# Kernel tuning notes

Measured on AMD Instinct MI355X. Metric: run time of the kernel, lower is better.

Reference implementation:

```python
import jax, jax.numpy as jnp
import numpy as np

N_NODES = 20000
STEPS = 10  # message_passing_steps


def _mlp(x, p):
    # 3-layer MLP: Linear->ReLU->Linear->ReLU->Linear (no final activation)
    W1, b1, W2, b2, W3, b3 = p
    h = jax.nn.relu(x @ W1 + b1)
    h = jax.nn.relu(h @ W2 + b2)
    return h @ W3 + b3


def _aggregate(dst, edge_attr, num_nodes):
    # scatter_add of edge features into destination nodes, degree-normalized (deg clamped to >=1)
    agg = jax.ops.segment_sum(edge_attr, dst, num_segments=num_nodes)
    deg = jax.ops.segment_sum(jnp.ones((dst.shape[0], 1), edge_attr.dtype), dst, num_segments=num_nodes)
    return agg / jnp.maximum(deg, 1.0)


def setup_inputs() -> dict:
    key = jax.random.key(0)
    N, EM, EC = N_NODES, 120000, 20000
    ND, MD, CD, OD, L = 12, 7, 4, 3, 128
    keys = iter(jax.random.split(key, 128))

    def lin(i, o):
        return (jax.random.normal(next(keys), (i, o), jnp.float32) * 0.05,
                jax.random.normal(next(keys), (o,), jnp.float32) * 0.05)

    inp = {
        "node_x": jax.random.normal(next(keys), (N, ND), jnp.float32),
        "mesh_edge_attr": jax.random.normal(next(keys), (EM, MD), jnp.float32),
        "contact_edge_attr": jax.random.normal(next(keys), (EC, CD), jnp.float32),
    }
    dims = {"ne": (ND, L), "me": (MD, L), "ce": (CD, L), "pe": (3 * L, L), "pn": (3 * L, L), "de": (L, OD)}
    for name, (i, o) in dims.items():
        W1, b1 = lin(i, L)
        W2, b2 = lin(L, L)
        W3, b3 = lin(L, o)
        for pn, p in zip(["W1", "b1", "W2", "b2", "W3", "b3"], [W1, b1, W2, b2, W3, b3]):
            inp[name + "_" + pn] = p
    inp["mesh_edge_index"] = jax.random.randint(next(keys), (2, EM), 0, N)
    inp["contact_edge_index"] = jax.random.randint(next(keys), (2, EC), 0, N)
    return inp


def reference(node_x, mesh_edge_attr, contact_edge_attr,
              ne_W1, ne_b1, ne_W2, ne_b2, ne_W3, ne_b3,
              me_W1, me_b1, me_W2, me_b2, me_W3, me_b3,
              ce_W1, ce_b1, ce_W2, ce_b2, ce_W3, ce_b3,
              pe_W1, pe_b1, pe_W2, pe_b2, pe_W3, pe_b3,
              pn_W1, pn_b1, pn_W2, pn_b2, pn_W3, pn_b3,
              de_W1, de_b1, de_W2, de_b2, de_W3, de_b3,
              mesh_edge_index, contact_edge_index):
    ne = (ne_W1, ne_b1, ne_W2, ne_b2, ne_W3, ne_b3)
    mep = (me_W1, me_b1, me_W2, me_b2, me_W3, me_b3)
    cep = (ce_W1, ce_b1, ce_W2, ce_b2, ce_W3, ce_b3)
    pe = (pe_W1, pe_b1, pe_W2, pe_b2, pe_W3, pe_b3)
    pn = (pn_W1, pn_b1, pn_W2, pn_b2, pn_W3, pn_b3)
    de = (de_W1, de_b1, de_W2, de_b2, de_W3, de_b3)
    N = node_x.shape[0]
    # encode
    x = _mlp(node_x, ne)                 # [N, 128]
    me = _mlp(mesh_edge_attr, mep)       # [EM, 128]
    ce = _mlp(contact_edge_attr, cep)    # [EC, 128]
    msrc, mdst = mesh_edge_index[0], mesh_edge_index[1]
    csrc, cdst = contact_edge_index[0], contact_edge_index[1]
    # process (shared edge_mlp for both edge types, residual updates)
    for _ in range(STEPS):
        me = me + _mlp(jnp.concatenate([x[msrc], x[mdst], me], axis=-1), pe)
        ce = ce + _mlp(jnp.concatenate([x[csrc], x[cdst], ce], axis=-1), pe)
        agg_m = _aggregate(mdst, me, N)
        agg_c = _aggregate(cdst, ce, N)
        x = x + _mlp(jnp.concatenate([x, agg_m, agg_c], axis=-1), pn)
    # decode
    return _mlp(x, de)                   # [N, 3]
```

## Files before the change

kernel.cpp:

```cpp
#include <hip/hip_runtime.h>
#include <stdint.h>

typedef unsigned short u16;
typedef __attribute__((ext_vector_type(8))) short bf16x8;
typedef __attribute__((ext_vector_type(4))) float f32x4;

#define NNODES 20000
#define EM 120000
#define EC 20000
#define LDIM 128
#define MT 32
#define MT2 64
#define A_STR 392
#define H_STR 136

__device__ __forceinline__ u16 f2bf(float f){
  uint32_t b = __float_as_uint(f);
  b += 0x7FFF + ((b >> 16) & 1);
  return (u16)(b >> 16);
}

template<int KB>
__device__ __forceinline__ void layer(const u16* sIn, int in_str, const u16* Wp,
                                      int wr, int wc, int lane, f32x4 acc[4]){
  const int row = wr*16 + (lane & 15);
  const int kg  = lane >> 4;
  #pragma unroll
  for (int kb = 0; kb < KB; ++kb){
    bf16x8 a = *(const bf16x8*)(sIn + row*in_str + kb*32 + kg*8);
    const u16* wb = Wp + (((kb*8 + wc*4)*64 + lane) << 3);
    #pragma unroll
    for (int nf = 0; nf < 4; ++nf){
      bf16x8 b = *(const bf16x8*)(wb + (nf << 9));
      acc[nf] = __builtin_amdgcn_mfma_f32_16x16x32_bf16(a, b, acc[nf], 0, 0, 0);
    }
  }
}

__device__ __forceinline__ void hid_epi(f32x4 acc[4], const float* bias,
                                        int wr, int wc, int lane, u16* sOut){
  const int cl = lane & 15;
  const int r0 = wr*16 + (lane >> 4)*4;
  #pragma unroll
  for (int nf = 0; nf < 4; ++nf){
    int col = wc*64 + nf*16 + cl;
    float bv = bias[col];
    #pragma unroll
    for (int r = 0; r < 4; ++r){
      float v = acc[nf][r] + bv;
      sOut[(r0 + r)*H_STR + col] = f2bf(v > 0.f ? v : 0.f);
    }
  }
}

__device__ __forceinline__ void zero4(f32x4 acc[4]){
  const f32x4 vz = {0.f, 0.f, 0.f, 0.f};
  #pragma unroll
  for (int i = 0; i < 4; ++i) acc[i] = vz;
}

template<int KB>
__device__ __forceinline__ void layer64(const u16* sIn, const u16* Wp,
                                        int wr, int wc, int lane, f32x4 acc[2][2]){
  const int r0 = wr*32 + (lane & 15);
  const int kg = lane >> 4;
  const u16* a0p = sIn + r0*A_STR + kg*8;
  const u16* a1p = a0p + 16*A_STR;
  const u16* wb  = Wp + (((wc*2)*64 + lane) << 3);
  #pragma unroll
  for (int kb = 0; kb < KB; ++kb){
    bf16x8 a0 = *(const bf16x8*)(a0p + kb*32);
    bf16x8 a1 = *(const bf16x8*)(a1p + kb*32);
    const u16* wk = wb + kb*4096;
    bf16x8 b0 = *(const bf16x8*)(wk);
    bf16x8 b1 = *(const bf16x8*)(wk + 512);
    acc[0][0] = __builtin_amdgcn_mfma_f32_16x16x32_bf16(a0, b0, acc[0][0], 0, 0, 0);
    acc[1][0] = __builtin_amdgcn_mfma_f32_16x16x32_bf16(a1, b0, acc[1][0], 0, 0, 0);
    acc[0][1] = __builtin_amdgcn_mfma_f32_16x16x32_bf16(a0, b1, acc[0][1], 0, 0, 0);
    acc[1][1] = __builtin_amdgcn_mfma_f32_16x16x32_bf16(a1, b1, acc[1][1], 0, 0, 0);
  }
}

__device__ __forceinline__ void hid_epi64(f32x4 acc[2][2], const float* bias,
                                          int wr, int wc, int lane, u16* sOut){
  const int cl = lane & 15;
  const int rq = (lane >> 4)*4;
  #pragma unroll
  for (int rf = 0; rf < 2; ++rf){
    int r0 = wr*32 + rf*16 + rq;
    #pragma unroll
    for (int nf = 0; nf < 2; ++nf){
      int col = wc*32 + nf*16 + cl;
      float bv = bias[col];
      #pragma unroll
      for (int r = 0; r < 4; ++r){
        float v = acc[rf][nf][r] + bv;
        sOut[(r0 + r)*A_STR + col] = f2bf(v > 0.f ? v : 0.f);
      }
    }
  }
}

__device__ __forceinline__ void zero22(f32x4 acc[2][2]){
  const f32x4 vz = {0.f, 0.f, 0.f, 0.f};
  acc[0][0] = vz; acc[0][1] = vz; acc[1][0] = vz; acc[1][1] = vz;
}

struct PackDesc { const float* src; int K_raw, N_raw, NF, elem_off; };
struct PackArgs { PackDesc d[18]; int total; };

__global__ __launch_bounds__(256) void pack_weights(PackArgs pa, u16* dst){
  int idx = blockIdx.x*256 + threadIdx.x;
  if (idx >= pa.total) return;
  int di = 0;
  #pragma unroll
  for (int i = 1; i < 18; ++i) if (idx >= pa.d[i].elem_off) di = i;
  PackDesc dd = pa.d[di];
  int e = idx - dd.elem_off;
  int f = e >> 9, lane = (e >> 3) & 63, j = e & 7;
  int kb = f / dd.NF, nf = f % dd.NF;
  int k = kb*32 + (lane >> 4)*8 + j;
  int n = nf*16 + (lane & 15);
  float v = (k < dd.K_raw && n < dd.N_raw) ? dd.src[k*dd.N_raw + n] : 0.f;
  dst[idx] = f2bf(v);
}

__global__ __launch_bounds__(256) void hist_kernel(const int* mdst, const int* cdst,
                                                   int* cnt_m, int* cnt_c){
  int i = blockIdx.x*256 + threadIdx.x;
  if (i < EM) atomicAdd(&cnt_m[mdst[i]], 1);
  else if (i < EM + EC) atomicAdd(&cnt_c[cdst[i - EM]], 1);
}

struct ScanArgs { const int *cnt_m, *cnt_c; int *start_m, *start_c, *cur_m, *cur_c; };

__global__ __launch_bounds__(256) void scan_kernel(ScanArgs a){
  const int n = NNODES;
  const int* cnt = blockIdx.x == 0 ? a.cnt_m : a.cnt_c;
  int* start     = blockIdx.x == 0 ? a.start_m : a.start_c;
  int* cur       = blockIdx.x == 0 ? a.cur_m : a.cur_c;
  __shared__ int part[256];
  __shared__ int base[257];
  int t = threadIdx.x;
  const int per = (n + 255) / 256;
  int lo = t*per, hi = min(n, lo + per);
  int s = 0;
  for (int j = lo; j < hi; ++j) s += cnt[j];
  part[t] = s;
  __syncthreads();
  if (t == 0){
    int run = 0;
    for (int i = 0; i < 256; ++i){ base[i] = run; run += part[i]; }
    base[256] = run;
  }
  __syncthreads();
  int run = base[t];
  for (int j = lo; j < hi; ++j){ start[j] = run; cur[j] = run; run += cnt[j]; }
  if (t == 255) start[n] = base[256];
}

__global__ __launch_bounds__(256) void scatter_kernel(const int* mdst, const int* cdst,
                                                      int* cur_m, int* cur_c,
                                                      int* eid_m, int* eid_c){
  int i = blockIdx.x*256 + threadIdx.x;
  if (i < EM){
    int p = atomicAdd(&cur_m[mdst[i]], 1);
    eid_m[p] = i;
  } else if (i < EM + EC){
    int e = i - EM;
    int p = atomicAdd(&cur_c[cdst[e]], 1);
    eid_c[p] = e;
  }
}

struct EncArgs {
  const float* in; int Kraw;
  const u16 *Wp1, *Wp2, *Wp3;
  const float *b1, *b2, *b3;
  float* out_f32; u16* out_b16;
};

__global__ __launch_bounds__(256) void enc_kernel(EncArgs a){
  __shared__ u16 sA[MT*A_STR];
  __shared__ u16 sH[MT*H_STR];
  const int tid = threadIdx.x, lane = tid & 63, w = tid >> 6, wr = w & 1, wc = w >> 1;
  const int m0 = blockIdx.x * MT;
  for (int i = tid; i < MT*32; i += 256){
    int row = i >> 5, c = i & 31;
    float v = (c < a.Kraw) ? a.in[(size_t)(m0 + row)*a.Kraw + c] : 0.f;
    sA[row*A_STR + c] = f2bf(v);
  }
  __syncthreads();
  f32x4 acc[4]; zero4(acc);
  layer<1>(sA, A_STR, a.Wp1, wr, wc, lane, acc);
  hid_epi(acc, a.b1, wr, wc, lane, sH);
  __syncthreads();
  zero4(acc);
  layer<4>(sH, H_STR, a.Wp2, wr, wc, lane, acc);
  hid_epi(acc, a.b2, wr, wc, lane, sA);
  __syncthreads();
  zero4(acc);
  layer<4>(sA, H_STR, a.Wp3, wr, wc, lane, acc);
  const int cl = lane & 15, r0l = wr*16 + (lane >> 4)*4;
  #pragma unroll
  for (int nf = 0; nf < 4; ++nf){
    int col = wc*64 + nf*16 + cl;
    float bv = a.b3[col];
    #pragma unroll
    for (int r = 0; r < 4; ++r){
      int m = m0 + r0l + r;
      float v = acc[nf][r] + bv;
      a.out_f32[(size_t)m*LDIM + col] = v;
      a.out_b16[(size_t)m*LDIM + col] = f2bf(v);
    }
  }
}

struct EdgeArgs {
  const u16 *Wp1, *Wp2, *Wp3;
  const float *b1, *b2, *b3;
  const u16* x_b16;
  const int *msrc, *mdst, *csrc, *cdst;
  u16 *me_b16, *ce_b16;
  float *me_f32, *ce_f32;
  int mesh_blocks;
};

__global__ __launch_bounds__(512) void edge_kernel(EdgeArgs a){
  __shared__ u16 sA[MT2*A_STR];
  const int tid = threadIdx.x, lane = tid & 63, w = tid >> 6, wr = w & 1, wc = w >> 1;
  const bool mesh = (int)blockIdx.x < a.mesh_blocks;
  const int e0 = (mesh ? (int)blockIdx.x : (int)blockIdx.x - a.mesh_blocks) * MT2;
  const int E = mesh ? EM : EC;
  const int* src = mesh ? a.msrc : a.csrc;
  const int* dst = mesh ? a.mdst : a.cdst;
  u16* fb   = mesh ? a.me_b16 : a.ce_b16;
  float* ff = mesh ? a.me_f32 : a.ce_f32;

  for (int i = tid; i < MT2*48; i += 512){
    int row = i/48, ch = i%48;
    int e = e0 + row; if (e >= E) e = E - 1;
    const u16* sp;
    if (ch < 16)       sp = a.x_b16 + (size_t)src[e]*LDIM + ch*8;
    else if (ch < 32)  sp = a.x_b16 + (size_t)dst[e]*LDIM + (ch-16)*8;
    else               sp = fb + (size_t)e*LDIM + (ch-32)*8;
    *(bf16x8*)(sA + row*A_STR + ch*8) = *(const bf16x8*)sp;
  }
  __syncthreads();
  f32x4 acc[2][2]; zero22(acc);
  layer64<12>(sA, a.Wp1, wr, wc, lane, acc);
  __syncthreads();
  hid_epi64(acc, a.b1, wr, wc, lane, sA + 256);
  __syncthreads();
  zero22(acc);
  layer64<4>(sA + 256, a.Wp2, wr, wc, lane, acc);
  hid_epi64(acc, a.b2, wr, wc, lane, sA);
  __syncthreads();
  zero22(acc);
  layer64<4>(sA, a.Wp3, wr, wc, lane, acc);

  const int cl = lane & 15, rq = (lane >> 4)*4;
  #pragma unroll
  for (int rf = 0; rf < 2; ++rf){
    #pragma unroll
    for (int r = 0; r < 4; ++r){
      int e = e0 + wr*32 + rf*16 + rq + r;
      if (e < E){
        #pragma unroll
        for (int nf = 0; nf < 2; ++nf){
          int col = wc*32 + nf*16 + cl;
          float nv = ff[(size_t)e*LDIM + col] + acc[rf][nf][r] + a.b3[col];
          ff[(size_t)e*LDIM + col] = nv;
          fb[(size_t)e*LDIM + col] = f2bf(nv);
        }
      }
    }
  }
}

struct NodeArgs {
  const u16 *Wp1, *Wp2, *Wp3;
  const float *b1, *b2, *b3;
  const u16* x_b16_in;
  const float *me_f32, *ce_f32;
  const int *start_m, *eid_m, *start_c, *eid_c;
  float* x_f32; u16* x_b16_out;
};

__global__ __launch_bounds__(512) void node_kernel(NodeArgs a){
  __shared__ u16 sA[MT2*A_STR];
  const int tid = threadIdx.x, lane = tid & 63, w = tid >> 6, wr = w & 1, wc = w >> 1;
  const int n0 = blockIdx.x * MT2;

  for (int i = tid; i < MT2*16; i += 512){
    int row = i >> 4, ch = i & 15;
    int n = n0 + row; if (n >= NNODES) n = NNODES - 1;
    *(bf16x8*)(sA + row*A_STR + ch*8) = *(const bf16x8*)(a.x_b16_in + (size_t)n*LDIM + ch*8);
  }

  {
    const int r = tid >> 3, c0 = (tid & 7) * 16;
    const int n = n0 + r;
    const bool ok = n < NNODES;
    {
      int s = ok ? a.start_m[n] : 0, e = ok ? a.start_m[n+1] : 0;
      f32x4 a0{0,0,0,0}, a1{0,0,0,0}, a2{0,0,0,0}, a3{0,0,0,0};
      for (int j = s; j < e; ++j){
        const f32x4* p = (const f32x4*)(a.me_f32 + (size_t)a.eid_m[j]*LDIM + c0);
        a0 += p[0]; a1 += p[1]; a2 += p[2]; a3 += p[3];
      }
      float inv = 1.f / fmaxf((float)(e - s), 1.f);
      bf16x8 t0, t1;
      #pragma unroll
      for (int k = 0; k < 4; ++k){
        t0[k]   = (short)f2bf(a0[k]*inv); t0[k+4] = (short)f2bf(a1[k]*inv);
        t1[k]   = (short)f2bf(a2[k]*inv); t1[k+4] = (short)f2bf(a3[k]*inv);
      }
      *(bf16x8*)(sA + r*A_STR + 128 + c0) = t0;
      *(bf16x8*)(sA + r*A_STR + 128 + c0 + 8) = t1;
    }
    {
      int s = ok ? a.start_c[n] : 0, e = ok ? a.start_c[n+1] : 0;
      f32x4 a0{0,0,0,0}, a1{0,0,0,0}, a2{0,0,0,0}, a3{0,0,0,0};
      for (int j = s; j < e; ++j){
        const f32x4* p = (const f32x4*)(a.ce_f32 + (size_t)a.eid_c[j]*LDIM + c0);
        a0 += p[0]; a1 += p[1]; a2 += p[2]; a3 += p[3];
      }
      float inv = 1.f / fmaxf((float)(e - s), 1.f);
      bf16x8 t0, t1;
      #pragma unroll
      for (int k = 0; k < 4; ++k){
        t0[k]   = (short)f2bf(a0[k]*inv); t0[k+4] = (short)f2bf(a1[k]*inv);
        t1[k]   = (short)f2bf(a2[k]*inv); t1[k+4] = (short)f2bf(a3[k]*inv);
      }
      *(bf16x8*)(sA + r*A_STR + 256 + c0) = t0;
      *(bf16x8*)(sA + r*A_STR + 256 + c0 + 8) = t1;
    }
  }
  __syncthreads();
  f32x4 acc[2][2]; zero22(acc);
  layer64<12>(sA, a.Wp1, wr, wc, lane, acc);
  __syncthreads();
  hid_epi64(acc, a.b1, wr, wc, lane, sA + 256);
  __syncthreads();
  zero22(acc);
  layer64<4>(sA + 256, a.Wp2, wr, wc, lane, acc);
  hid_epi64(acc, a.b2, wr, wc, lane, sA);
  __syncthreads();
  zero22(acc);
  layer64<4>(sA, a.Wp3, wr, wc, lane, acc);

  const int cl = lane & 15, rq = (lane >> 4)*4;
  #pragma unroll
  for (int rf = 0; rf < 2; ++rf){
    #pragma unroll
    for (int r = 0; r < 4; ++r){
      int n = n0 + wr*32 + rf*16 + rq + r;
      if (n < NNODES){
        #pragma unroll
        for (int nf = 0; nf < 2; ++nf){
          int col = wc*32 + nf*16 + cl;
          float nv = a.x_f32[(size_t)n*LDIM + col] + acc[rf][nf][r] + a.b3[col];
          a.x_f32[(size_t)n*LDIM + col] = nv;
          a.x_b16_out[(size_t)n*LDIM + col] = f2bf(nv);
        }
      }
    }
  }
}

struct DecArgs {
  const u16 *Wp1, *Wp2, *Wp3;
  const float *b1, *b2, *b3;
  const u16* x_b16; float* out;
};

__global__ __launch_bounds__(256) void dec_kernel(DecArgs a){
  __shared__ u16 sA[MT*A_STR];
  __shared__ u16 sH[MT*H_STR];
  const int tid = threadIdx.x, lane = tid & 63, w = tid >> 6, wr = w & 1, wc = w >> 1;
  const int n0 = blockIdx.x * MT;
  for (int i = tid; i < MT*16; i += 256){
    int row = i >> 4, ch = i & 15;
    *(bf16x8*)(sA + row*H_STR + ch*8) = *(const bf16x8*)(a.x_b16 + (size_t)(n0+row)*LDIM + ch*8);
  }
  __syncthreads();
  f32x4 acc[4]; zero4(acc);
  layer<4>(sA, H_STR, a.Wp1, wr, wc, lane, acc);
  hid_epi(acc, a.b1, wr, wc, lane, sH);
  __syncthreads();
  zero4(acc);
  layer<4>(sH, H_STR, a.Wp2, wr, wc, lane, acc);
  hid_epi(acc, a.b2, wr, wc, lane, sA);
  __syncthreads();
  if (wc == 0){
    f32x4 a3 = {0.f, 0.f, 0.f, 0.f};
    const int row = wr*16 + (lane & 15), kg = lane >> 4;
    #pragma unroll
    for (int kb = 0; kb < 4; ++kb){
      bf16x8 av = *(const bf16x8*)(sA + row*H_STR + kb*32 + kg*8);
      bf16x8 bv = *(const bf16x8*)(a.Wp3 + ((kb*64 + lane) << 3));
      a3 = __builtin_amdgcn_mfma_f32_16x16x32_bf16(av, bv, a3, 0, 0, 0);
    }
    const int cl = lane & 15, r0l = wr*16 + (lane >> 4)*4;
    if (cl < 3){
      #pragma unroll
      for (int r = 0; r < 4; ++r)
        a.out[(size_t)(n0 + r0l + r)*3 + cl] = a3[r] + a.b3[cl];
    }
  }
}

extern "C" void kernel_launch(void* const* d_in, const int* in_sizes, int n_in,
                              void* d_out, int out_size, void* d_ws, size_t ws_size,
                              hipStream_t stream){
  auto F = [&](int i){ return (const float*)d_in[i]; };
  const float* node_x   = F(0);
  const float* mesh_attr = F(1);
  const float* cont_attr = F(2);
  const int* mei = (const int*)d_in[39];
  const int* cei = (const int*)d_in[40];
  const int *msrc = mei, *mdst = mei + EM, *csrc = cei, *cdst = cei + EC;

  char* ws = (char*)d_ws;
  size_t off = 0;
  auto take = [&](size_t b)->void*{ void* p = ws + off; off += (b + 255) & ~(size_t)255; return p; };
  float* x_f32  = (float*)take((size_t)NNODES*LDIM*4);
  u16*   x_b16  = (u16*)  take((size_t)NNODES*LDIM*2);
  float* me_f32 = (float*)take((size_t)EM*LDIM*4);
  u16*   me_b16 = (u16*)  take((size_t)EM*LDIM*2);
  float* ce_f32 = (float*)take((size_t)EC*LDIM*4);
  u16*   ce_b16 = (u16*)  take((size_t)EC*LDIM*2);
  u16*   wpack  = (u16*)  take((size_t)309248*2);
  int* cnt_m   = (int*)take((size_t)NNODES*4);
  int* cnt_c   = (int*)take((size_t)NNODES*4);
  int* start_m = (int*)take((size_t)(NNODES+1)*4);
  int* start_c = (int*)take((size_t)(NNODES+1)*4);
  int* cur_m   = (int*)take((size_t)NNODES*4);
  int* cur_c   = (int*)take((size_t)NNODES*4);
  int* eid_m   = (int*)take((size_t)EM*4);
  int* eid_c   = (int*)take((size_t)EC*4);

  static const int tbl[18][5] = {
    {3,12,128,32,128},{5,128,128,128,128},{7,128,128,128,128},
    {9,7,128,32,128},{11,128,128,128,128},{13,128,128,128,128},
    {15,4,128,32,128},{17,128,128,128,128},{19,128,128,128,128},
    {21,384,128,384,128},{23,128,128,128,128},{25,128,128,128,128},
    {27,384,128,384,128},{29,128,128,128,128},{31,128,128,128,128},
    {33,128,128,128,128},{35,128,128,128,128},{37,128,3,128,16}};
  PackArgs pa; int eo = 0; int offs[18];
  for (int i = 0; i < 18; ++i){
    offs[i] = eo;
    pa.d[i].src = F(tbl[i][0]);
    pa.d[i].K_raw = tbl[i][1];
    pa.d[i].N_raw = tbl[i][2];
    pa.d[i].NF = tbl[i][4] / 16;
    pa.d[i].elem_off = eo;
    eo += tbl[i][3] * tbl[i][4];
  }
  pa.total = eo;
  pack_weights<<<dim3(eo/256), dim3(256), 0, stream>>>(pa, wpack);

  size_t cnt_span = ((char*)cnt_c - (char*)cnt_m) + (size_t)NNODES*4;
  hipMemsetAsync(cnt_m, 0, cnt_span, stream);
  hist_kernel<<<dim3((EM + EC + 255)/256), dim3(256), 0, stream>>>(mdst, cdst, cnt_m, cnt_c);
  ScanArgs sa{cnt_m, cnt_c, start_m, start_c, cur_m, cur_c};
  scan_kernel<<<dim3(2), dim3(256), 0, stream>>>(sa);
  scatter_kernel<<<dim3((EM + EC + 255)/256), dim3(256), 0, stream>>>(mdst, cdst, cur_m, cur_c, eid_m, eid_c);

  EncArgs en{node_x, 12, wpack+offs[0], wpack+offs[1], wpack+offs[2], F(4), F(6), F(8), x_f32, x_b16};
  enc_kernel<<<dim3(NNODES/MT), dim3(256), 0, stream>>>(en);
  EncArgs em{mesh_attr, 7, wpack+offs[3], wpack+offs[4], wpack+offs[5], F(10), F(12), F(14), me_f32, me_b16};
  enc_kernel<<<dim3(EM/MT), dim3(256), 0, stream>>>(em);
  EncArgs ec{cont_attr, 4, wpack+offs[6], wpack+offs[7], wpack+offs[8], F(16), F(18), F(20), ce_f32, ce_b16};
  enc_kernel<<<dim3(EC/MT), dim3(256), 0, stream>>>(ec);

  EdgeArgs ea;
  ea.Wp1 = wpack+offs[9]; ea.Wp2 = wpack+offs[10]; ea.Wp3 = wpack+offs[11];
  ea.b1 = F(22); ea.b2 = F(24); ea.b3 = F(26);
  ea.x_b16 = x_b16;
  ea.msrc = msrc; ea.mdst = mdst; ea.csrc = csrc; ea.cdst = cdst;
  ea.me_b16 = me_b16; ea.ce_b16 = ce_b16;
  ea.me_f32 = me_f32; ea.ce_f32 = ce_f32;
  ea.mesh_blocks = EM/MT2;

  NodeArgs na;
  na.Wp1 = wpack+offs[12]; na.Wp2 = wpack+offs[13]; na.Wp3 = wpack+offs[14];
  na.b1 = F(28); na.b2 = F(30); na.b3 = F(32);
  na.x_b16_in = x_b16;
  na.me_f32 = me_f32; na.ce_f32 = ce_f32;
  na.start_m = start_m; na.eid_m = eid_m; na.start_c = start_c; na.eid_c = eid_c;
  na.x_f32 = x_f32; na.x_b16_out = x_b16;

  const int edge_blocks = EM/MT2 + (EC + MT2 - 1)/MT2;
  const int node_blocks = (NNODES + MT2 - 1)/MT2;
  for (int s = 0; s < 10; ++s){
    edge_kernel<<<dim3(edge_blocks), dim3(512), 0, stream>>>(ea);
    node_kernel<<<dim3(node_blocks), dim3(512), 0, stream>>>(na);
  }

  DecArgs da{wpack+offs[15], wpack+offs[16], wpack+offs[17], F(34), F(36), F(38), x_b16, (float*)d_out};
  dec_kernel<<<dim3(NNODES/MT), dim3(256), 0, stream>>>(da);
}
```

Baseline: 1.230 ms.

## Gather node features directly into MFMA registers and drop bf16 edge copies

The edge and node kernels now load the gathered x[src]/x[dst] (and x for nodes) rows straight from global memory into MFMA A-operands, rather than staging them in a large shared tile. Only the edge state (converted from f32 to bf16 on load) and the aggregates go through shared memory. The separate bf16 copies of the edge features are removed, so the f32 edge state is the only one written each step. Shared memory per block shrinks and launch bounds request more resident blocks, at the cost of uncoalesced per-lane global gathers inside the K loop and an f32 read plus conversion per step.

```diff
diff --git a/kernel.cpp b/kernel.cpp
--- a/kernel.cpp
+++ b/kernel.cpp
@@ -13,11 +13,16 @@
 #define MT2 64
 #define A_STR 392
 #define H_STR 136
+#define G_STR 264
 
 __device__ __forceinline__ u16 f2bf(float f){
   uint32_t b = __float_as_uint(f);
   b += 0x7FFF + ((b >> 16) & 1);
   return (u16)(b >> 16);
+}
+
+__device__ __forceinline__ f32x4 mfma16(bf16x8 a, bf16x8 b, f32x4 c){
+  return __builtin_amdgcn_mfma_f32_16x16x32_bf16(a, b, c, 0, 0, 0);
 }
 
 template<int KB>
@@ -32,7 +37,7 @@
     #pragma unroll
     for (int nf = 0; nf < 4; ++nf){
       bf16x8 b = *(const bf16x8*)(wb + (nf << 9));
-      acc[nf] = __builtin_amdgcn_mfma_f32_16x16x32_bf16(a, b, acc[nf], 0, 0, 0);
+      acc[nf] = mfma16(a, b, acc[nf]);
     }
   }
 }
@@ -59,13 +64,13 @@
   for (int i = 0; i < 4; ++i) acc[i] = vz;
 }
 
-template<int KB>
+template<int KB, int STR>
 __device__ __forceinline__ void layer64(const u16* sIn, const u16* Wp,
                                         int wr, int wc, int lane, f32x4 acc[2][2]){
   const int r0 = wr*32 + (lane & 15);
   const int kg = lane >> 4;
-  const u16* a0p = sIn + r0*A_STR + kg*8;
-  const u16* a1p = a0p + 16*A_STR;
+  const u16* a0p = sIn + r0*STR + kg*8;
+  const u16* a1p = a0p + 16*STR;
   const u16* wb  = Wp + (((wc*2)*64 + lane) << 3);
   #pragma unroll
   for (int kb = 0; kb < KB; ++kb){
@@ -74,13 +79,14 @@
     const u16* wk = wb + kb*4096;
     bf16x8 b0 = *(const bf16x8*)(wk);
     bf16x8 b1 = *(const bf16x8*)(wk + 512);
-    acc[0][0] = __builtin_amdgcn_mfma_f32_16x16x32_bf16(a0, b0, acc[0][0], 0, 0, 0);
-    acc[1][0] = __builtin_amdgcn_mfma_f32_16x16x32_bf16(a1, b0, acc[1][0], 0, 0, 0);
-    acc[0][1] = __builtin_amdgcn_mfma_f32_16x16x32_bf16(a0, b1, acc[0][1], 0, 0, 0);
-    acc[1][1] = __builtin_amdgcn_mfma_f32_16x16x32_bf16(a1, b1, acc[1][1], 0, 0, 0);
-  }
-}
-
+    acc[0][0] = mfma16(a0, b0, acc[0][0]);
+    acc[1][0] = mfma16(a1, b0, acc[1][0]);
+    acc[0][1] = mfma16(a0, b1, acc[0][1]);
+    acc[1][1] = mfma16(a1, b1, acc[1][1]);
+  }
+}
+
+template<int STR>
 __device__ __forceinline__ void hid_epi64(f32x4 acc[2][2], const float* bias,
                                           int wr, int wc, int lane, u16* sOut){
   const int cl = lane & 15;
@@ -95,7 +101,7 @@
       #pragma unroll
       for (int r = 0; r < 4; ++r){
         float v = acc[rf][nf][r] + bv;
-        sOut[(r0 + r)*A_STR + col] = f2bf(v > 0.f ? v : 0.f);
+        sOut[(r0 + r)*STR + col] = f2bf(v > 0.f ? v : 0.f);
       }
     }
   }
@@ -211,7 +217,7 @@
       int m = m0 + r0l + r;
       float v = acc[nf][r] + bv;
       a.out_f32[(size_t)m*LDIM + col] = v;
-      a.out_b16[(size_t)m*LDIM + col] = f2bf(v);
+      if (a.out_b16) a.out_b16[(size_t)m*LDIM + col] = f2bf(v);
     }
   }
 }
@@ -221,43 +227,73 @@
   const float *b1, *b2, *b3;
   const u16* x_b16;
   const int *msrc, *mdst, *csrc, *cdst;
-  u16 *me_b16, *ce_b16;
   float *me_f32, *ce_f32;
   int mesh_blocks;
 };
 
-__global__ __launch_bounds__(512) void edge_kernel(EdgeArgs a){
-  __shared__ u16 sA[MT2*A_STR];
+__global__ __launch_bounds__(512, 8) void edge_kernel(EdgeArgs a){
+  __shared__ u16 sB0[MT2*H_STR];
+  __shared__ u16 sB1[MT2*H_STR];
   const int tid = threadIdx.x, lane = tid & 63, w = tid >> 6, wr = w & 1, wc = w >> 1;
   const bool mesh = (int)blockIdx.x < a.mesh_blocks;
   const int e0 = (mesh ? (int)blockIdx.x : (int)blockIdx.x - a.mesh_blocks) * MT2;
   const int E = mesh ? EM : EC;
   const int* src = mesh ? a.msrc : a.csrc;
   const int* dst = mesh ? a.mdst : a.cdst;
-  u16* fb   = mesh ? a.me_b16 : a.ce_b16;
   float* ff = mesh ? a.me_f32 : a.ce_f32;
 
-  for (int i = tid; i < MT2*48; i += 512){
-    int row = i/48, ch = i%48;
+  const int r0 = wr*32 + (lane & 15);
+  int eA = e0 + r0;      if (eA >= E) eA = E - 1;
+  int eB = e0 + r0 + 16; if (eB >= E) eB = E - 1;
+  const int sA_ = src[eA], sB_ = src[eB], dA_ = dst[eA], dB_ = dst[eB];
+
+  #pragma unroll
+  for (int t = tid; t < MT2*16; t += 512){
+    int row = t >> 4, ch = t & 15;
     int e = e0 + row; if (e >= E) e = E - 1;
-    const u16* sp;
-    if (ch < 16)       sp = a.x_b16 + (size_t)src[e]*LDIM + ch*8;
-    else if (ch < 32)  sp = a.x_b16 + (size_t)dst[e]*LDIM + (ch-16)*8;
-    else               sp = fb + (size_t)e*LDIM + (ch-32)*8;
-    *(bf16x8*)(sA + row*A_STR + ch*8) = *(const bf16x8*)sp;
-  }
-  __syncthreads();
+    const float* sp = ff + (size_t)e*LDIM + ch*8;
+    bf16x8 v;
+    #pragma unroll
+    for (int j = 0; j < 8; ++j) v[j] = (short)f2bf(sp[j]);
+    *(bf16x8*)(sB0 + row*H_STR + ch*8) = v;
+  }
+  __syncthreads();
+
   f32x4 acc[2][2]; zero22(acc);
-  layer64<12>(sA, a.Wp1, wr, wc, lane, acc);
-  __syncthreads();
-  hid_epi64(acc, a.b1, wr, wc, lane, sA + 256);
+  {
+    const int cb = (lane >> 4)*8;
+    const u16* wb = a.Wp1 + (((wc*2)*64 + lane) << 3);
+    #pragma unroll
+    for (int kb = 0; kb < 12; ++kb){
+      bf16x8 a0, a1;
+      if (kb < 4){
+        a0 = *(const bf16x8*)(a.x_b16 + (size_t)sA_*LDIM + kb*32 + cb);
+        a1 = *(const bf16x8*)(a.x_b16 + (size_t)sB_*LDIM + kb*32 + cb);
+      } else if (kb < 8){
+        a0 = *(const bf16x8*)(a.x_b16 + (size_t)dA_*LDIM + (kb-4)*32 + cb);
+        a1 = *(const bf16x8*)(a.x_b16 + (size_t)dB_*LDIM + (kb-4)*32 + cb);
+      } else {
+        a0 = *(const bf16x8*)(sB0 + r0*H_STR + (kb-8)*32 + cb);
+        a1 = *(const bf16x8*)(sB0 + (r0+16)*H_STR + (kb-8)*32 + cb);
+      }
+      const u16* wk = wb + kb*4096;
+      bf16x8 b0 = *(const bf16x8*)(wk);
+      bf16x8 b1 = *(const bf16x8*)(wk + 512);
+      acc[0][0] = mfma16(a0, b0, acc[0][0]);
+      acc[1][0] = mfma16(a1, b0, acc[1][0]);
+      acc[0][1] = mfma16(a0, b1, acc[0][1]);
+      acc[1][1] = mfma16(a1, b1, acc[1][1]);
+    }
+  }
+  __syncthreads();
+  hid_epi64<H_STR>(acc, a.b1, wr, wc, lane, sB1);
   __syncthreads();
   zero22(acc);
-  layer64<4>(sA + 256, a.Wp2, wr, wc, lane, acc);
-  hid_epi64(acc, a.b2, wr, wc, lane, sA);
+  layer64<4, H_STR>(sB1, a.Wp2, wr, wc, lane, acc);
+  hid_epi64<H_STR>(acc, a.b2, wr, wc, lane, sB0);
   __syncthreads();
   zero22(acc);
-  layer64<4>(sA, a.Wp3, wr, wc, lane, acc);
+  layer64<4, H_STR>(sB0, a.Wp3, wr, wc, lane, acc);
 
   const int cl = lane & 15, rq = (lane >> 4)*4;
   #pragma unroll
@@ -271,7 +307,6 @@
           int col = wc*32 + nf*16 + cl;
           float nv = ff[(size_t)e*LDIM + col] + acc[rf][nf][r] + a.b3[col];
           ff[(size_t)e*LDIM + col] = nv;
-          fb[(size_t)e*LDIM + col] = f2bf(nv);
         }
       }
     }
@@ -287,16 +322,10 @@
   float* x_f32; u16* x_b16_out;
 };
 
-__global__ __launch_bounds__(512) void node_kernel(NodeArgs a){
-  __shared__ u16 sA[MT2*A_STR];
+__global__ __launch_bounds__(512, 8) void node_kernel(NodeArgs a){
+  __shared__ u16 sG[MT2*G_STR];
   const int tid = threadIdx.x, lane = tid & 63, w = tid >> 6, wr = w & 1, wc = w >> 1;
   const int n0 = blockIdx.x * MT2;
-
-  for (int i = tid; i < MT2*16; i += 512){
-    int row = i >> 4, ch = i & 15;
-    int n = n0 + row; if (n >= NNODES) n = NNODES - 1;
-    *(bf16x8*)(sA + row*A_STR + ch*8) = *(const bf16x8*)(a.x_b16_in + (size_t)n*LDIM + ch*8);
-  }
 
   {
     const int r = tid >> 3, c0 = (tid & 7) * 16;
@@ -316,8 +345,8 @@
         t0[k]   = (short)f2bf(a0[k]*inv); t0[k+4] = (short)f2bf(a1[k]*inv);
         t1[k]   = (short)f2bf(a2[k]*inv); t1[k+4] = (short)f2bf(a3[k]*inv);
       }
-      *(bf16x8*)(sA + r*A_STR + 128 + c0) = t0;
-      *(bf16x8*)(sA + r*A_STR + 128 + c0 + 8) = t1;
+      *(bf16x8*)(sG + r*G_STR + c0) = t0;
+      *(bf16x8*)(sG + r*G_STR + c0 + 8) = t1;
     }
     {
       int s = ok ? a.start_c[n] : 0, e = ok ? a.start_c[n+1] : 0;
@@ -333,22 +362,48 @@
         t0[k]   = (short)f2bf(a0[k]*inv); t0[k+4] = (short)f2bf(a1[k]*inv);
         t1[k]   = (short)f2bf(a2[k]*inv); t1[k+4] = (short)f2bf(a3[k]*inv);
       }
-      *(bf16x8*)(sA + r*A_STR + 256 + c0) = t0;
-      *(bf16x8*)(sA + r*A_STR + 256 + c0 + 8) = t1;
-    }
-  }
-  __syncthreads();
+      *(bf16x8*)(sG + r*G_STR + 128 + c0) = t0;
+      *(bf16x8*)(sG + r*G_STR + 128 + c0 + 8) = t1;
+    }
+  }
+  __syncthreads();
+
+  const int r0 = wr*32 + (lane & 15);
+  int nA = n0 + r0;      if (nA >= NNODES) nA = NNODES - 1;
+  int nB = n0 + r0 + 16; if (nB >= NNODES) nB = NNODES - 1;
+
   f32x4 acc[2][2]; zero22(acc);
-  layer64<12>(sA, a.Wp1, wr, wc, lane, acc);
-  __syncthreads();
-  hid_epi64(acc, a.b1, wr, wc, lane, sA + 256);
+  {
+    const int cb = (lane >> 4)*8;
+    const u16* wb = a.Wp1 + (((wc*2)*64 + lane) << 3);
+    #pragma unroll
+    for (int kb = 0; kb < 12; ++kb){
+      bf16x8 a0, a1;
+      if (kb < 4){
+        a0 = *(const bf16x8*)(a.x_b16_in + (size_t)nA*LDIM + kb*32 + cb);
+        a1 = *(const bf16x8*)(a.x_b16_in + (size_t)nB*LDIM + kb*32 + cb);
+      } else {
+        a0 = *(const bf16x8*)(sG + r0*G_STR + (kb-4)*32 + cb);
+        a1 = *(const bf16x8*)(sG + (r0+16)*G_STR + (kb-4)*32 + cb);
+      }
+      const u16* wk = wb + kb*4096;
+      bf16x8 b0 = *(const bf16x8*)(wk);
+      bf16x8 b1 = *(const bf16x8*)(wk + 512);
+      acc[0][0] = mfma16(a0, b0, acc[0][0]);
+      acc[1][0] = mfma16(a1, b0, acc[1][0]);
+      acc[0][1] = mfma16(a0, b1, acc[0][1]);
+      acc[1][1] = mfma16(a1, b1, acc[1][1]);
+    }
+  }
+  __syncthreads();
+  hid_epi64<G_STR>(acc, a.b1, wr, wc, lane, sG);
   __syncthreads();
   zero22(acc);
-  layer64<4>(sA + 256, a.Wp2, wr, wc, lane, acc);
-  hid_epi64(acc, a.b2, wr, wc, lane, sA);
+  layer64<4, G_STR>(sG, a.Wp2, wr, wc, lane, acc);
+  hid_epi64<G_STR>(acc, a.b2, wr, wc, lane, sG + 128);
   __syncthreads();
   zero22(acc);
-  layer64<4>(sA, a.Wp3, wr, wc, lane, acc);
+  layer64<4, G_STR>(sG + 128, a.Wp3, wr, wc, lane, acc);
 
   const int cl = lane & 15, rq = (lane >> 4)*4;
   #pragma unroll
@@ -400,7 +455,7 @@
     for (int kb = 0; kb < 4; ++kb){
       bf16x8 av = *(const bf16x8*)(sA + row*H_STR + kb*32 + kg*8);
       bf16x8 bv = *(const bf16x8*)(a.Wp3 + ((kb*64 + lane) << 3));
-      a3 = __builtin_amdgcn_mfma_f32_16x16x32_bf16(av, bv, a3, 0, 0, 0);
+      a3 = mfma16(av, bv, a3);
     }
     const int cl = lane & 15, r0l = wr*16 + (lane >> 4)*4;
     if (cl < 3){
@@ -428,9 +483,7 @@
   float* x_f32  = (float*)take((size_t)NNODES*LDIM*4);
   u16*   x_b16  = (u16*)  take((size_t)NNODES*LDIM*2);
   float* me_f32 = (float*)take((size_t)EM*LDIM*4);
-  u16*   me_b16 = (u16*)  take((size_t)EM*LDIM*2);
   float* ce_f32 = (float*)take((size_t)EC*LDIM*4);
-  u16*   ce_b16 = (u16*)  take((size_t)EC*LDIM*2);
   u16*   wpack  = (u16*)  take((size_t)309248*2);
   int* cnt_m   = (int*)take((size_t)NNODES*4);
   int* cnt_c   = (int*)take((size_t)NNODES*4);
@@ -470,9 +523,9 @@
 
   EncArgs en{node_x, 12, wpack+offs[0], wpack+offs[1], wpack+offs[2], F(4), F(6), F(8), x_f32, x_b16};
   enc_kernel<<<dim3(NNODES/MT), dim3(256), 0, stream>>>(en);
-  EncArgs em{mesh_attr, 7, wpack+offs[3], wpack+offs[4], wpack+offs[5], F(10), F(12), F(14), me_f32, me_b16};
+  EncArgs em{mesh_attr, 7, wpack+offs[3], wpack+offs[4], wpack+offs[5], F(10), F(12), F(14), me_f32, nullptr};
   enc_kernel<<<dim3(EM/MT), dim3(256), 0, stream>>>(em);
-  EncArgs ec{cont_attr, 4, wpack+offs[6], wpack+offs[7], wpack+offs[8], F(16), F(18), F(20), ce_f32, ce_b16};
+  EncArgs ec{cont_attr, 4, wpack+offs[6], wpack+offs[7], wpack+offs[8], F(16), F(18), F(20), ce_f32, nullptr};
   enc_kernel<<<dim3(EC/MT), dim3(256), 0, stream>>>(ec);
 
   EdgeArgs ea;
@@ -480,7 +533,6 @@
   ea.b1 = F(22); ea.b2 = F(24); ea.b3 = F(26);
   ea.x_b16 = x_b16;
   ea.msrc = msrc; ea.mdst = mdst; ea.csrc = csrc; ea.cdst = cdst;
-  ea.me_b16 = me_b16; ea.ce_b16 = ce_b16;
   ea.me_f32 = me_f32; ea.ce_f32 = ce_f32;
   ea.mesh_blocks = EM/MT2;
 
```

New measurement: 1.345 ms. 9.3% more time.
